# Kernel tuning notes

Measured on AMD Instinct MI355X. Metric: run time of the kernel, lower is better.

Reference implementation:

```python
import jax, jax.numpy as jnp
import numpy as np

EPS = 1e-3  # Keras BatchNormalization default epsilon
HEADS = 4
KEY_DEPTH = 16   # k
INTRA = 1        # u
VAL_DEPTH = 64   # v = kernel_out // heads = 256 // 4
C_IN = 256
B, HH, WW = 16, 32, 32
N = HH * WW      # == size of positional embedding


def setup_inputs() -> dict:
    key = jax.random.key(0)
    ks = jax.random.split(key, 6)
    x = jax.random.normal(ks[0], (B, HH, WW, C_IN), dtype=jnp.float32)
    # 1x1 conv kernels == dense matrices over the channel dim
    Wq = jax.random.normal(ks[1], (C_IN, KEY_DEPTH * HEADS), dtype=jnp.float32) * 0.05
    Wk = jax.random.normal(ks[2], (C_IN, KEY_DEPTH * INTRA), dtype=jnp.float32) * 0.05
    Wv = jax.random.normal(ks[3], (C_IN, VAL_DEPTH * INTRA), dtype=jnp.float32) * 0.05
    # BatchNorm (inference mode) parameters
    gamma_q = jnp.ones((KEY_DEPTH * HEADS,), jnp.float32)
    beta_q = jnp.zeros((KEY_DEPTH * HEADS,), jnp.float32)
    mean_q = jnp.zeros((KEY_DEPTH * HEADS,), jnp.float32)
    var_q = jnp.ones((KEY_DEPTH * HEADS,), jnp.float32)
    gamma_v = jnp.ones((VAL_DEPTH * INTRA,), jnp.float32)
    beta_v = jnp.zeros((VAL_DEPTH * INTRA,), jnp.float32)
    mean_v = jnp.zeros((VAL_DEPTH * INTRA,), jnp.float32)
    var_v = jnp.ones((VAL_DEPTH * INTRA,), jnp.float32)
    # Positional embedding: [size, size, key_depth, intra_depth], uniform init
    E = jax.random.uniform(ks[4], (N, N, KEY_DEPTH, INTRA), dtype=jnp.float32)
    return {
        'x': x, 'Wq': Wq, 'Wk': Wk, 'Wv': Wv,
        'gamma_q': gamma_q, 'beta_q': beta_q, 'mean_q': mean_q, 'var_q': var_q,
        'gamma_v': gamma_v, 'beta_v': beta_v, 'mean_v': mean_v, 'var_v': var_v,
        'E': E,
    }


def _bn(t, gamma, beta, mean, var):
    return gamma * (t - mean) / jnp.sqrt(var + EPS) + beta


def reference(x, Wq, Wk, Wv, gamma_q, beta_q, mean_q, var_q,
              gamma_v, beta_v, mean_v, var_v, E):
    b, hh, ww, _ = x.shape
    n = hh * ww
    # 1x1 conv projections (context c == x)
    q = jnp.einsum('bhwc,cd->bhwd', x, Wq)           # [b,hh,ww,h*k]
    k = jnp.einsum('bhwc,cd->bhwd', x, Wk)           # [b,hh,ww,u*k]
    v = jnp.einsum('bhwc,cd->bhwd', x, Wv)           # [b,hh,ww,u*v]
    q = _bn(q, gamma_q, beta_q, mean_q, var_q)
    v = _bn(v, gamma_v, beta_v, mean_v, var_v)
    # softmax over the channel axis (faithful to the source code)
    k = jax.nn.softmax(k, axis=-1)
    # rearranges: b hh ww (h k) -> b h k n ; b hh ww (u k) -> b u k n ; b hh ww (u v) -> b u v n
    q = q.reshape(b, n, HEADS, KEY_DEPTH).transpose(0, 2, 3, 1)   # [b,h,k,n]
    k = k.reshape(b, n, INTRA, KEY_DEPTH).transpose(0, 2, 3, 1)   # [b,u,k,n]
    v = v.reshape(b, n, INTRA, VAL_DEPTH).transpose(0, 2, 3, 1)   # [b,u,v,n]
    # content lambda: sum over intra-depth and positions
    lam_c = jnp.einsum('bukn,buvn->bkv', k, v)                    # [b,k,v]
    Yc = jnp.einsum('bhkn,bkv->bhvn', q, lam_c)                   # [b,h,v,n]
    # positional lambdas: E[n,m,k,u] contracted with v[b,u,v,m]
    lam_p = jnp.einsum('nmku,buvm->bnkv', E, v)                   # [b,n,k,v]
    Yp = jnp.einsum('bhkn,bnkv->bhvn', q, lam_p)                  # [b,h,v,n]
    Y = Yc + Yp                                                    # [b,h,v,n]
    # b h v n -> b hh ww (h v)
    out = Y.transpose(0, 3, 1, 2).reshape(b, hh, ww, HEADS * VAL_DEPTH)
    return out
```

## Files before the change

kernel.cpp:

```cpp
#include <hip/hip_runtime.h>
#include <stdint.h>

#define EPS 1e-3f

typedef __bf16 bf16x8 __attribute__((ext_vector_type(8)));
typedef float  f32x4  __attribute__((ext_vector_type(4)));

static __device__ __forceinline__ uint16_t f2bf(float f) {
  union { __bf16 b; uint16_t u; } r; r.b = (__bf16)f; return r.u;
}
static __device__ __forceinline__ uint32_t cvt2(float lo, float hi) {
  union { __bf16 b[2]; uint32_t u; } r;
  r.b[0] = (__bf16)lo; r.b[1] = (__bf16)hi;
  return r.u;
}
static __device__ __forceinline__ void gload_lds16(const void* g, void* l) {
  __builtin_amdgcn_global_load_lds(
      (const __attribute__((address_space(1))) unsigned int*)g,
      (__attribute__((address_space(3))) unsigned int*)l, 16, 0, 0);
}

__global__ __launch_bounds__(256) void wprep(
    const float* __restrict__ Wq, const float* __restrict__ Wk,
    const float* __restrict__ Wv, uint16_t* __restrict__ WtP)
{
  const int col = blockIdx.x, t = threadIdx.x;
  float val = (col < 64) ? Wq[t * 64 + col]
            : (col < 80) ? Wk[t * 16 + (col - 64)]
                         : Wv[t * 64 + (col - 80)];
  WtP[col * 264 + t] = f2bf(val);
}

__global__ __launch_bounds__(256) void proj_mfma(
    const float* __restrict__ x, const uint16_t* __restrict__ WtP,
    const float* __restrict__ gq, const float* __restrict__ bq,
    const float* __restrict__ mq, const float* __restrict__ vq,
    const float* __restrict__ gv, const float* __restrict__ bv,
    const float* __restrict__ mv, const float* __restrict__ vvp,
    float* __restrict__ Qf, uint16_t* __restrict__ VbfT,
    float* __restrict__ part)
{
  __shared__ __align__(16) char smem[111616];
  uint16_t* const xA = (uint16_t*)smem;
  char* const Wt = smem + 33792;

  const int t = threadIdx.x;
  const int wid = t >> 6, lane = t & 63;
  const int bid = blockIdx.x;
  const int b = bid >> 4, mc = bid & 15;
  const int r0 = b * 1024 + mc * 64;

#pragma unroll
  for (int i = 0; i < 19; ++i) {
    int off = (i * 256 + t) * 16;
    gload_lds16((const char*)WtP + off, Wt + off);
  }
  {
    const int row = t >> 2, ks0 = (t & 3) * 64;
    const float* src = x + (size_t)(r0 + row) * 256 + ks0;
    uint16_t* dstp = xA + row * 264 + ks0;
#pragma unroll
    for (int i = 0; i < 8; ++i) {
      float4 d0 = *(const float4*)(src + i * 8);
      float4 d1 = *(const float4*)(src + i * 8 + 4);
      uint4 q;
      q.x = cvt2(d0.x, d0.y); q.y = cvt2(d0.z, d0.w);
      q.z = cvt2(d1.x, d1.y); q.w = cvt2(d1.z, d1.w);
      *(uint4*)(dstp + i * 8) = q;
    }
  }
  __syncthreads();

  f32x4 acc[9];
#pragma unroll
  for (int f = 0; f < 9; ++f) acc[f] = f32x4{0.f, 0.f, 0.f, 0.f};
  const int arow = wid * 16 + (lane & 15);
#pragma unroll
  for (int kst = 0; kst < 8; ++kst) {
    const int sb = kst * 64 + ((lane >> 4) << 4);
    bf16x8 af = *(const bf16x8*)((const char*)xA + arow * 528 + sb);
#pragma unroll
    for (int f = 0; f < 9; ++f) {
      const int crow = f * 16 + (lane & 15);
      bf16x8 bfr = *(const bf16x8*)(Wt + crow * 528 + sb);
      acc[f] = __builtin_amdgcn_mfma_f32_16x16x32_bf16(af, bfr, acc[f], 0, 0, 0);
    }
  }

  const int cl = lane & 15;
  const int rbase = wid * 16 + ((lane >> 4) << 2);

  float qs[4], qb[4], qm[4], vs[4], vb[4], vm[4];
#pragma unroll
  for (int f = 0; f < 4; ++f) {
    const int c = f * 16 + cl;
    qs[f] = gq[c] * rsqrtf(vq[c] + EPS); qb[f] = bq[c]; qm[f] = mq[c];
    vs[f] = gv[c] * rsqrtf(vvp[c] + EPS); vb[f] = bv[c]; vm[f] = mv[c];
  }
#pragma unroll
  for (int f = 0; f < 4; ++f)
#pragma unroll
    for (int r = 0; r < 4; ++r)
      Qf[(size_t)(r0 + rbase + r) * 64 + f * 16 + cl] =
          (acc[f][r] - qm[f]) * qs[f] + qb[f];
  float ex[4];
#pragma unroll
  for (int r = 0; r < 4; ++r) {
    float kv = acc[4][r];
    float mx = kv;
#pragma unroll
    for (int d = 1; d < 16; d <<= 1) mx = fmaxf(mx, __shfl_xor(mx, d, 64));
    float e = __expf(kv - mx);
    float sm = e;
#pragma unroll
    for (int d = 1; d < 16; d <<= 1) sm += __shfl_xor(sm, d, 64);
    ex[r] = e / sm;
  }
  float vv[4][4];
#pragma unroll
  for (int f = 0; f < 4; ++f)
#pragma unroll
    for (int r = 0; r < 4; ++r)
      vv[f][r] = (acc[5 + f][r] - vm[f]) * vs[f] + vb[f];

  __syncthreads();
  float* const vt = (float*)smem;
  float* const ks = (float*)(smem + 64 * 65 * 4);
#pragma unroll
  for (int r = 0; r < 4; ++r) ks[(rbase + r) * 20 + cl] = ex[r];
#pragma unroll
  for (int f = 0; f < 4; ++f)
#pragma unroll
    for (int r = 0; r < 4; ++r) vt[(rbase + r) * 65 + f * 16 + cl] = vv[f][r];
  __syncthreads();

  {
    const int v = t & 63, grp = t >> 6;
#pragma unroll
    for (int h = 0; h < 2; ++h) {
      uint4 q;
      q.x = cvt2(vt[(grp * 16 + h * 8 + 0) * 65 + v], vt[(grp * 16 + h * 8 + 1) * 65 + v]);
      q.y = cvt2(vt[(grp * 16 + h * 8 + 2) * 65 + v], vt[(grp * 16 + h * 8 + 3) * 65 + v]);
      q.z = cvt2(vt[(grp * 16 + h * 8 + 4) * 65 + v], vt[(grp * 16 + h * 8 + 5) * 65 + v]);
      q.w = cvt2(vt[(grp * 16 + h * 8 + 6) * 65 + v], vt[(grp * 16 + h * 8 + 7) * 65 + v]);
      *(uint4*)&VbfT[(size_t)(b * 64 + v) * 1024 + mc * 64 + grp * 16 + h * 8] = q;
    }
  }
  {
    const int kq = t >> 6, v = t & 63;
    float a0 = 0.f, a1 = 0.f, a2 = 0.f, a3 = 0.f;
#pragma unroll 4
    for (int m = 0; m < 64; ++m) {
      float vvx = vt[m * 65 + v];
      a0 = fmaf(ks[m * 20 + kq * 4 + 0], vvx, a0);
      a1 = fmaf(ks[m * 20 + kq * 4 + 1], vvx, a1);
      a2 = fmaf(ks[m * 20 + kq * 4 + 2], vvx, a2);
      a3 = fmaf(ks[m * 20 + kq * 4 + 3], vvx, a3);
    }
    float* dst = part + ((size_t)(b * 16 + mc) << 10) + (kq * 4) * 64 + v;
    dst[0] = a0; dst[64] = a1; dst[128] = a2; dst[192] = a3;
  }
}

__global__ __launch_bounds__(256) void lamc_reduce(const float* __restrict__ part,
                                                   float* __restrict__ Lc)
{
  const int gid = blockIdx.x * 256 + threadIdx.x;
  const int b = gid >> 10, r = gid & 1023;
  const float* p = part + ((size_t)b << 14) + r;
  float s = 0.f;
#pragma unroll
  for (int mc = 0; mc < 16; ++mc) s += p[mc << 10];
  Lc[((size_t)b << 10) + r] = s;
}

__global__ __launch_bounds__(1024, 4) void gemm_out(
    const float* __restrict__ E,
    const uint16_t* __restrict__ VbfT,
    const float* __restrict__ Qf,
    const float* __restrict__ Lc,
    float* __restrict__ out)
{
  __shared__ __align__(16) char smem[131072];
  char* const A0 = smem;
  char* const B0 = smem + 32768;
  char* const A1 = smem + 65536;
  char* const B1 = smem + 98304;

  const int t = threadIdx.x;
  const int wid = t >> 6, lane = t & 63;
  const int wm = wid >> 2, wn = wid & 3;
  const int bid = blockIdx.x;
  const int xcd = bid & 7, idx = bid >> 3;
  const int rb = xcd * 8 + (idx >> 2);
  const int cb = idx & 3;
  const int col0 = cb * 256;
  const int n0 = rb * 16;
  const int b0i = cb * 4;

  const int kq = t & 3;
  const int mp = (t >> 2) & 31;
  const int nb = t >> 7;
  const float* Eb = E + ((size_t)n0 << 14);

  int awoff[2][4];
#pragma unroll
  for (int it = 0; it < 2; ++it)
#pragma unroll
    for (int j = 0; j < 4; ++j) {
      int row = (it * 8 + nb) * 16 + kq * 4 + j;
      awoff[it][j] = row * 128 + ((mp * 4) ^ ((row & 7) << 4));
    }

  const uint16_t* bptr[2];
  int bdst[2];
  {
    const uint16_t* Bb = VbfT + ((size_t)col0 << 10);
#pragma unroll
    for (int it = 0; it < 2; ++it) {
      int id = it * 1024 + t;
      int row = id >> 3, seg = id & 7;
      bptr[it] = Bb + (row << 10) + ((seg ^ (row & 7)) << 3);
      bdst[it] = id * 16;
    }
  }

  f32x4 acc[4][4];
  {
    const int bb = b0i + wn;
    const float* lb = Lc + (size_t)(((bb << 4) + ((lane >> 4) << 2)) << 6);
#pragma unroll
    for (int j = 0; j < 4; ++j) {
      const int v = j * 16 + (lane & 15);
      f32x4 lc;
#pragma unroll
      for (int r = 0; r < 4; ++r) lc[r] = lb[(r << 6) + v];
#pragma unroll
      for (int i = 0; i < 4; ++i) acc[i][j] = lc;
    }
  }

  float4 ra[2], rbx[2];

#pragma unroll
  for (int it = 0; it < 2; ++it) {
    size_t base = ((size_t)(it * 8 + nb) << 14) + ((size_t)(mp * 2) << 4) + (kq << 2);
    ra[it]  = *(const float4*)(Eb + base);
    rbx[it] = *(const float4*)(Eb + base + 16);
  }
#pragma unroll
  for (int it = 0; it < 2; ++it) gload_lds16(bptr[it], B0 + bdst[it]);
#pragma unroll
  for (int it = 0; it < 2; ++it) {
    const float* da = (const float*)&ra[it];
    const float* db = (const float*)&rbx[it];
#pragma unroll
    for (int j = 0; j < 4; ++j)
      *(uint32_t*)(A0 + awoff[it][j]) = cvt2(da[j], db[j]);
  }
  __syncthreads();

#pragma unroll 1
  for (int kt = 0; kt < 16; ++kt) {
    char* Ac = (kt & 1) ? A1 : A0;
    char* Bc = (kt & 1) ? B1 : B0;
    char* An = (kt & 1) ? A0 : A1;
    char* Bn = (kt & 1) ? B0 : B1;
    if (kt < 15) {
      const int m0n = (kt + 1) * 64;
#pragma unroll
      for (int it = 0; it < 2; ++it) {
        size_t base = ((size_t)(it * 8 + nb) << 14) +
                      ((size_t)(m0n + mp * 2) << 4) + (kq << 2);
        ra[it]  = *(const float4*)(Eb + base);
        rbx[it] = *(const float4*)(Eb + base + 16);
      }
#pragma unroll
      for (int it = 0; it < 2; ++it) gload_lds16(bptr[it] + m0n, Bn + bdst[it]);
    }
    __builtin_amdgcn_s_setprio(1);
#pragma unroll
    for (int kk = 0; kk < 2; ++kk) {
      bf16x8 a[4], b[4];
      const int s = kk * 4 + (lane >> 4);
#pragma unroll
      for (int i = 0; i < 4; ++i) {
        int row = wm * 64 + i * 16 + (lane & 15);
        a[i] = *(const bf16x8*)(Ac + row * 128 + ((s ^ (row & 7)) << 4));
      }
#pragma unroll
      for (int j = 0; j < 4; ++j) {
        int row = wn * 64 + j * 16 + (lane & 15);
        b[j] = *(const bf16x8*)(Bc + row * 128 + ((s ^ (row & 7)) << 4));
      }
#pragma unroll
      for (int i = 0; i < 4; ++i)
#pragma unroll
        for (int j = 0; j < 4; ++j)
          acc[i][j] = __builtin_amdgcn_mfma_f32_16x16x32_bf16(a[i], b[j], acc[i][j], 0, 0, 0);
    }
    __builtin_amdgcn_s_setprio(0);
    if (kt < 15) {
#pragma unroll
      for (int it = 0; it < 2; ++it) {
        const float* da = (const float*)&ra[it];
        const float* db = (const float*)&rbx[it];
#pragma unroll
        for (int j = 0; j < 4; ++j)
          *(uint32_t*)(An + awoff[it][j]) = cvt2(da[j], db[j]);
      }
    }
    __syncthreads();
  }

  float* Cs = (float*)smem;
#pragma unroll
  for (int p = 0; p < 4; ++p) {
    if (wm == p) {
#pragma unroll
      for (int i = 0; i < 4; ++i) {
#pragma unroll
        for (int j = 0; j < 4; ++j) {
          const int col = wn * 64 + j * 16 + (lane & 15);
#pragma unroll
          for (int r = 0; r < 4; ++r) {
            const int rl = i * 16 + ((lane >> 4) << 2) + r;
            Cs[rl * 258 + col] = acc[i][j][r];
          }
        }
      }
    }
    __syncthreads();
    {
      const int v = t & 63;
#pragma unroll
      for (int c = 0; c < 4; ++c) {
        const int combo = ((t >> 6) << 2) + c;
        const int n_l = combo >> 4;
        const int b_l = (combo >> 2) & 3;
        const int h = combo & 3;
        const int n = n0 + (p << 2) + n_l;
        const int bb = b0i + b_l;
        const float* qp = Qf + (((size_t)(bb << 10) + n) << 6) + (h << 4);
        float sum = 0.f;
#pragma unroll
        for (int k = 0; k < 16; ++k)
          sum = fmaf(qp[k], Cs[((n_l << 4) + k) * 258 + (b_l << 6) + v], sum);
        out[(((size_t)(bb << 10) + n) << 8) + (h << 6) + v] = sum;
      }
    }
    __syncthreads();
  }
}

extern "C" void kernel_launch(void* const* d_in, const int* in_sizes, int n_in,
                              void* d_out, int out_size, void* d_ws, size_t ws_size,
                              hipStream_t stream) {
  const float* x   = (const float*)d_in[0];
  const float* Wq  = (const float*)d_in[1];
  const float* Wk  = (const float*)d_in[2];
  const float* Wv  = (const float*)d_in[3];
  const float* gq  = (const float*)d_in[4];
  const float* bq  = (const float*)d_in[5];
  const float* mq  = (const float*)d_in[6];
  const float* vq  = (const float*)d_in[7];
  const float* gv  = (const float*)d_in[8];
  const float* bv  = (const float*)d_in[9];
  const float* mv  = (const float*)d_in[10];
  const float* vvp = (const float*)d_in[11];
  const float* E   = (const float*)d_in[12];
  float* out = (float*)d_out;

  char* ws = (char*)d_ws;
  uint16_t* VbfT = (uint16_t*)(ws);
  float*    Qf   = (float*)(ws + (size_t)(2 << 20));
  float*    part = (float*)(ws + (size_t)(6 << 20));
  float*    Lc   = (float*)(ws + (size_t)(7 << 20));
  uint16_t* WtP  = (uint16_t*)(ws + (size_t)(7 << 20) + 65536);

  hipLaunchKernelGGL(wprep, dim3(144), dim3(256), 0, stream, Wq, Wk, Wv, WtP);
  hipLaunchKernelGGL(proj_mfma, dim3(256), dim3(256), 0, stream, x, WtP,
                     gq, bq, mq, vq, gv, bv, mv, vvp, Qf, VbfT, part);
  hipLaunchKernelGGL(lamc_reduce, dim3(64), dim3(256), 0, stream, part, Lc);
  hipLaunchKernelGGL(gemm_out, dim3(256), dim3(1024), 0, stream, E, VbfT, Qf, Lc, out);
}
```

Measured before the change: 67.40 us.

## Halve K-tile and LDS footprint in gemm_out to fit two blocks per CU

Shrinks the gemm_out double-buffered LDS tiles from 128 KB to 64 KB by halving the K-step from 64 to 32, which doubles the loop trip count to 32. The swizzle pattern is redone for 64-byte rows, and the per-lane LDS offsets are precomputed once. The launch bound is lowered to 2 waves per SIMD so that two 1024-thread blocks can share a CU. The epilogue is restaged in eight smaller passes so its tile fits the smaller LDS. The goal is better latency hiding through a second resident block, paid for with more barriers per unit of work and a longer epilogue.

```diff
diff --git a/kernel.cpp b/kernel.cpp
--- a/kernel.cpp
+++ b/kernel.cpp
@@ -174,18 +174,18 @@
   Lc[((size_t)b << 10) + r] = s;
 }
 
-__global__ __launch_bounds__(1024, 4) void gemm_out(
+__global__ __launch_bounds__(1024, 2) void gemm_out(
     const float* __restrict__ E,
     const uint16_t* __restrict__ VbfT,
     const float* __restrict__ Qf,
     const float* __restrict__ Lc,
     float* __restrict__ out)
 {
-  __shared__ __align__(16) char smem[131072];
+  __shared__ __align__(16) char smem[65536];
   char* const A0 = smem;
+  char* const A1 = smem + 16384;
   char* const B0 = smem + 32768;
-  char* const A1 = smem + 65536;
-  char* const B1 = smem + 98304;
+  char* const B1 = smem + 49152;
 
   const int t = threadIdx.x;
   const int wid = t >> 6, lane = t & 63;
@@ -199,30 +199,33 @@
   const int b0i = cb * 4;
 
   const int kq = t & 3;
-  const int mp = (t >> 2) & 31;
-  const int nb = t >> 7;
-  const float* Eb = E + ((size_t)n0 << 14);
-
-  int awoff[2][4];
-#pragma unroll
-  for (int it = 0; it < 2; ++it)
-#pragma unroll
-    for (int j = 0; j < 4; ++j) {
-      int row = (it * 8 + nb) * 16 + kq * 4 + j;
-      awoff[it][j] = row * 128 + ((mp * 4) ^ ((row & 7) << 4));
-    }
-
-  const uint16_t* bptr[2];
-  int bdst[2];
-  {
-    const uint16_t* Bb = VbfT + ((size_t)col0 << 10);
-#pragma unroll
-    for (int it = 0; it < 2; ++it) {
-      int id = it * 1024 + t;
-      int row = id >> 3, seg = id & 7;
-      bptr[it] = Bb + (row << 10) + ((seg ^ (row & 7)) << 3);
-      bdst[it] = id * 16;
-    }
+  const int mp = (t >> 2) & 15;
+  const int nl = t >> 6;
+  const float* Eb = E + ((size_t)(n0 + nl) << 14);
+
+  int awoff[4];
+#pragma unroll
+  for (int j = 0; j < 4; ++j) {
+    int row = nl * 16 + kq * 4 + j;
+    int g = (mp >> 2) ^ ((row >> 1) & 3);
+    awoff[j] = row * 64 + (g << 4) + (mp & 3) * 4;
+  }
+
+  const int brow = t >> 2, bseg = t & 3;
+  const uint16_t* bptr = VbfT + ((size_t)(col0 + brow) << 10)
+                         + ((bseg ^ ((brow >> 1) & 3)) << 3);
+  const int bdst = t * 16;
+
+  int aoff[4], boff[4];
+#pragma unroll
+  for (int i = 0; i < 4; ++i) {
+    int r = wm * 64 + i * 16 + (lane & 15);
+    aoff[i] = r * 64 + (((lane >> 4) ^ ((r >> 1) & 3)) << 4);
+  }
+#pragma unroll
+  for (int j = 0; j < 4; ++j) {
+    int r = wn * 64 + j * 16 + (lane & 15);
+    boff[j] = r * 64 + (((lane >> 4) ^ ((r >> 1) & 3)) << 4);
   }
 
   f32x4 acc[4][4];
@@ -240,91 +243,73 @@
     }
   }
 
-  float4 ra[2], rbx[2];
-
-#pragma unroll
-  for (int it = 0; it < 2; ++it) {
-    size_t base = ((size_t)(it * 8 + nb) << 14) + ((size_t)(mp * 2) << 4) + (kq << 2);
-    ra[it]  = *(const float4*)(Eb + base);
-    rbx[it] = *(const float4*)(Eb + base + 16);
-  }
-#pragma unroll
-  for (int it = 0; it < 2; ++it) gload_lds16(bptr[it], B0 + bdst[it]);
-#pragma unroll
-  for (int it = 0; it < 2; ++it) {
-    const float* da = (const float*)&ra[it];
-    const float* db = (const float*)&rbx[it];
+  float4 ra, rbx;
+
+  {
+    const float* p = Eb + (size_t)(2 * mp) * 16 + kq * 4;
+    ra  = *(const float4*)p;
+    rbx = *(const float4*)(p + 16);
+  }
+  gload_lds16(bptr, B0 + bdst);
+  {
+    const float* da = (const float*)&ra;
+    const float* db = (const float*)&rbx;
 #pragma unroll
     for (int j = 0; j < 4; ++j)
-      *(uint32_t*)(A0 + awoff[it][j]) = cvt2(da[j], db[j]);
+      *(uint32_t*)(A0 + awoff[j]) = cvt2(da[j], db[j]);
   }
   __syncthreads();
 
 #pragma unroll 1
-  for (int kt = 0; kt < 16; ++kt) {
+  for (int kt = 0; kt < 32; ++kt) {
     char* Ac = (kt & 1) ? A1 : A0;
     char* Bc = (kt & 1) ? B1 : B0;
     char* An = (kt & 1) ? A0 : A1;
     char* Bn = (kt & 1) ? B0 : B1;
-    if (kt < 15) {
-      const int m0n = (kt + 1) * 64;
-#pragma unroll
-      for (int it = 0; it < 2; ++it) {
-        size_t base = ((size_t)(it * 8 + nb) << 14) +
-                      ((size_t)(m0n + mp * 2) << 4) + (kq << 2);
-        ra[it]  = *(const float4*)(Eb + base);
-        rbx[it] = *(const float4*)(Eb + base + 16);
-      }
-#pragma unroll
-      for (int it = 0; it < 2; ++it) gload_lds16(bptr[it] + m0n, Bn + bdst[it]);
-    }
-    __builtin_amdgcn_s_setprio(1);
-#pragma unroll
-    for (int kk = 0; kk < 2; ++kk) {
+    if (kt < 31) {
+      const int m0n = (kt + 1) * 32;
+      const float* p = Eb + (size_t)(m0n + 2 * mp) * 16 + kq * 4;
+      ra  = *(const float4*)p;
+      rbx = *(const float4*)(p + 16);
+      gload_lds16(bptr + m0n, Bn + bdst);
+    }
+    {
       bf16x8 a[4], b[4];
-      const int s = kk * 4 + (lane >> 4);
-#pragma unroll
-      for (int i = 0; i < 4; ++i) {
-        int row = wm * 64 + i * 16 + (lane & 15);
-        a[i] = *(const bf16x8*)(Ac + row * 128 + ((s ^ (row & 7)) << 4));
-      }
-#pragma unroll
-      for (int j = 0; j < 4; ++j) {
-        int row = wn * 64 + j * 16 + (lane & 15);
-        b[j] = *(const bf16x8*)(Bc + row * 128 + ((s ^ (row & 7)) << 4));
-      }
+#pragma unroll
+      for (int i = 0; i < 4; ++i) a[i] = *(const bf16x8*)(Ac + aoff[i]);
+#pragma unroll
+      for (int j = 0; j < 4; ++j) b[j] = *(const bf16x8*)(Bc + boff[j]);
+      __builtin_amdgcn_s_setprio(1);
 #pragma unroll
       for (int i = 0; i < 4; ++i)
 #pragma unroll
         for (int j = 0; j < 4; ++j)
           acc[i][j] = __builtin_amdgcn_mfma_f32_16x16x32_bf16(a[i], b[j], acc[i][j], 0, 0, 0);
-    }
-    __builtin_amdgcn_s_setprio(0);
-    if (kt < 15) {
-#pragma unroll
-      for (int it = 0; it < 2; ++it) {
-        const float* da = (const float*)&ra[it];
-        const float* db = (const float*)&rbx[it];
-#pragma unroll
-        for (int j = 0; j < 4; ++j)
-          *(uint32_t*)(An + awoff[it][j]) = cvt2(da[j], db[j]);
-      }
+      __builtin_amdgcn_s_setprio(0);
+    }
+    if (kt < 31) {
+      const float* da = (const float*)&ra;
+      const float* db = (const float*)&rbx;
+#pragma unroll
+      for (int j = 0; j < 4; ++j)
+        *(uint32_t*)(An + awoff[j]) = cvt2(da[j], db[j]);
     }
     __syncthreads();
   }
 
   float* Cs = (float*)smem;
 #pragma unroll
-  for (int p = 0; p < 4; ++p) {
-    if (wm == p) {
-#pragma unroll
-      for (int i = 0; i < 4; ++i) {
+  for (int p = 0; p < 8; ++p) {
+    if (wm == (p >> 1)) {
+#pragma unroll
+      for (int il = 0; il < 2; ++il) {
+        const int i = ((p & 1) << 1) + il;
 #pragma unroll
         for (int j = 0; j < 4; ++j) {
           const int col = wn * 64 + j * 16 + (lane & 15);
 #pragma unroll
           for (int r = 0; r < 4; ++r) {
-            const int rl = i * 16 + ((lane >> 4) << 2) + r;
+            const int rl = il * 16 + ((lane >> 4) << 2) + r;
             Cs[rl * 258 + col] = acc[i][j][r];
           }
         }
@@ -332,14 +317,13 @@
     }
     __syncthreads();
     {
-      const int v = t & 63;
-#pragma unroll
-      for (int c = 0; c < 4; ++c) {
-        const int combo = ((t >> 6) << 2) + c;
-        const int n_l = combo >> 4;
-        const int b_l = (combo >> 2) & 3;
-        const int h = combo & 3;
-        const int n = n0 + (p << 2) + n_l;
+      const int v = t & 63, g = t >> 6;
+#pragma unroll
+      for (int c = 0; c < 2; ++c) {
+        const int n_l = c;
+        const int b_l = g >> 2;
+        const int h = g & 3;
+        const int n = n0 + (p << 1) + n_l;
         const int bb = b0i + b_l;
         const float* qp = Qf + (((size_t)(bb << 10) + n) << 6) + (h << 4);
         float sum = 0.f;
```

Result: slower. 74.03 us (+9.8%).
